# Kernel tuning notes

Measured on AMD Instinct MI355X. Metric: run time of the kernel, lower is better.

The kernel has to match this reference:

```python
import jax, jax.numpy as jnp
import numpy as np

CELU_ALPHA = 0.1  # torchani standard CELU alpha


def _celu(x):
    return jax.nn.celu(x, alpha=CELU_ALPHA)


def setup_inputs() -> dict:
    key = jax.random.key(0)
    ks = jax.random.split(key, 12)
    N, S, E, D = 20000, 4, 8, 1008
    dims = [D, 256, 192, 160, 1]
    inp = {
        "aev": jax.random.normal(ks[0], (N, D), jnp.float32),
        "species": jax.random.randint(ks[1], (N,), 0, S, dtype=jnp.int64),
    }
    for l in range(4):
        din, dout = dims[l], dims[l + 1]
        inp[f"W{l}"] = jax.random.normal(ks[2 + 2 * l], (S, E, din, dout), jnp.float32) * (1.0 / np.sqrt(din).astype(np.float32))
        inp[f"b{l}"] = jax.random.normal(ks[3 + 2 * l], (S, E, dout), jnp.float32) * 0.05
    return inp


def reference(aev, species, W0, b0, W1, b1, W2, b2, W3, b3):
    # Faithful math of InferModel.forward: for each species i, gather atoms of
    # that species, run the BmmAtomicNetwork (ensemble of MLPs via bmm, CELU
    # activations, mean over ensemble members), sum per-species energies, then
    # sum into a single [1]-shaped total energy.
    # JIT-friendly equivalent: evaluate every species network on all atoms
    # (S=4 is small) and select each atom's output by its species index.
    # h: [S, E, N, hidden]
    h = _celu(jnp.einsum('ni,seio->seno', aev, W0) + b0[:, :, None, :])
    h = _celu(jnp.einsum('seni,seio->seno', h, W1) + b1[:, :, None, :])
    h = _celu(jnp.einsum('seni,seio->seno', h, W2) + b2[:, :, None, :])
    h = jnp.einsum('seni,seio->seno', h, W3) + b3[:, :, None, :]  # [S,E,N,1]
    per_atom = h.mean(axis=1)[:, :, 0]  # mean over ensemble -> [S, N]
    sel = jnp.take_along_axis(per_atom, species[None, :], axis=0)[0]  # [N]
    return jnp.sum(sel, keepdims=True)  # shape [1], total energy
```

## Files before the change

kernel.cpp:

```cpp
#include <hip/hip_runtime.h>
#include <cmath>

#define NA 20000
#define NS 4
#define NE 8
#define DD 1008
#define BM 128
#define MAXT 157
#define MAXROWS 20608

typedef unsigned short u16;
typedef unsigned int u32;
typedef unsigned long long u64;
typedef u16 u16x8 __attribute__((ext_vector_type(8)));
typedef u16 u16x4 __attribute__((ext_vector_type(4)));
typedef float f32x4 __attribute__((ext_vector_type(4)));
typedef short s16x8 __attribute__((ext_vector_type(8)));

__device__ __forceinline__ float bf2f(u16 h) {
  u32 u = ((u32)h) << 16;
  return __builtin_bit_cast(float, u);
}
__device__ __forceinline__ u16 f2bf(float f) {
  u32 b = __builtin_bit_cast(u32, f);
  u32 lsb = (b >> 16) & 1;
  return (u16)((b + 0x7fffu + lsb) >> 16);
}
__device__ __forceinline__ float celu_f(float x) {
#if __has_builtin(__builtin_amdgcn_exp2f)
  float e = __builtin_amdgcn_exp2f(x * 14.426950408889634f);
#else
  float e = exp2f(x * 14.426950408889634f);
#endif
  return x > 0.f ? x : 0.1f * (e - 1.f);
}
__device__ __forceinline__ float gf(const void* g, size_t i, bool isF32) {
  return isF32 ? ((const float*)g)[i] : bf2f(((const u16*)g)[i]);
}

__device__ __forceinline__ void gll16(const void* g, const u16* lds) {
#if __has_builtin(__builtin_amdgcn_global_load_lds)
  __builtin_amdgcn_global_load_lds(
      (const __attribute__((address_space(1))) u32*)g,
      (__attribute__((address_space(3))) u32*)(u16*)lds, 16, 0, 0);
#else
  int l = threadIdx.x & 63;
  *(f32x4*)((u16*)lds + l * 8) = *(const f32x4*)g;
#endif
}

#define CHUNK_BARRIER(N)                                   \
  do {                                                     \
    asm volatile("s_waitcnt vmcnt(" #N ")" ::: "memory");  \
    __builtin_amdgcn_sched_barrier(0);                     \
    __builtin_amdgcn_s_barrier();                          \
    __builtin_amdgcn_sched_barrier(0);                     \
  } while (0)

__global__ void k_probe0(const void* __restrict__ aev, const void* __restrict__ species,
                         int* __restrict__ w) {
  __shared__ int sh[2];
  int tid = threadIdx.x;
  if (tid < 64) w[tid] = 0;
  if (tid == 0) { sh[0] = 0; sh[1] = 0; }
  __syncthreads();
  const u16* a = (const u16*)aev;
  int bad = 0;
  for (int i = 0; i < 16; ++i) {
    u16 h = a[tid * 16 + i];
    int ex = (h >> 7) & 0xFF;
    if (ex < 107 || ex > 147) ++bad;
  }
  atomicAdd(&sh[0], bad);
  const int* sp = (const int*)species;
  int odd = 0;
  for (int i = 0; i < 4; ++i)
    if (sp[(tid * 4 + i) * 2 + 1] != 0) ++odd;
  atomicAdd(&sh[1], odd);
  __syncthreads();
  if (tid == 0) {
    w[18] = (sh[0] > 400) ? 1 : 0;
    w[19] = (sh[1] == 0) ? 1 : 0;
  }
}

__device__ __forceinline__ int get_species(const void* sp, int i, bool i64) {
  int s = i64 ? ((const int*)sp)[2 * i] : ((const int*)sp)[i];
  return s < 0 ? 0 : (s > 3 ? 3 : s);
}

__global__ void k_count(const void* __restrict__ species, int* __restrict__ w) {
  int i = blockIdx.x * 256 + threadIdx.x;
  int lane = threadIdx.x & 63;
  int s = (i < NA) ? get_species(species, i, w[19] != 0) : -1;
  for (int sp = 0; sp < 4; ++sp) {
    u64 m = __ballot(s == sp);
    if (m != 0 && lane == (__ffsll((long long)m) - 1))
      atomicAdd(&w[sp], __popcll(m));
  }
  __syncthreads();
  if (threadIdx.x == 0) {
    __threadfence();
    if (atomicAdd(&w[25], 1) == (int)gridDim.x - 1) {
      int b = 0, pb = 0;
      for (int sp = 0; sp < 4; ++sp) {
        int c = atomicAdd(&w[sp], 0);
        w[13 + sp] = b; b += c;
        w[20 + sp] = pb; pb += ((c + 127) >> 7) << 7;
      }
      w[24] = pb;
    }
  }
}

__global__ void k_scatsml(const void* __restrict__ species, int* __restrict__ w,
                          int* __restrict__ order,
                          const void* b0, const void* b1, const void* b2, const void* b3,
                          const void* W3, u16* ob0, u16* ob1, u16* ob2, u16* ob3,
                          u16* oW3, u16* gap) {
  if (blockIdx.x == 79) {
    const bool isF32 = (w[18] != 0);
    int t = threadIdx.x;
    for (int i = t; i < 32 * 256; i += 256) ob0[i] = f2bf(gf(b0, i, isF32));
    for (int i = t; i < 32 * 192; i += 256) ob1[i] = f2bf(gf(b1, i, isF32));
    for (int i = t; i < 32 * 160; i += 256) ob2[i] = f2bf(gf(b2, i, isF32));
    for (int i = t; i < 32 * 160; i += 256) oW3[i] = f2bf(gf(W3, i, isF32));
    if (t < 32) ob3[t] = f2bf(gf(b3, t, isF32));
    u16x8 z = {0, 0, 0, 0, 0, 0, 0, 0};
    *(u16x8*)(gap + t * 8) = z;
    return;
  }
  int i = blockIdx.x * 256 + threadIdx.x;
  int lane = threadIdx.x & 63;
  int s = (i < NA) ? get_species(species, i, w[19] != 0) : -1;
  for (int sp = 0; sp < 4; ++sp) {
    u64 m = __ballot(s == sp);
    if (m == 0) continue;
    int leader = __ffsll((long long)m) - 1;
    int base = 0;
    if (lane == leader) base = atomicAdd(&w[4 + sp], __popcll(m));
    base = __shfl(base, leader);
    if (s == sp) {
      int rank = __popcll(m & ((lane == 63) ? 0x7fffffffffffffffULL : ((1ULL << lane) - 1)));
      order[w[13 + sp] + base + rank] = i;
    }
  }
}

__global__ void k_gather(const void* __restrict__ aev, const int* __restrict__ w,
                         const int* __restrict__ order, u16* __restrict__ aevb) {
  const bool isF32 = (w[18] != 0);
  const int t = threadIdx.x;
  const int r = blockIdx.x * 4 + (t >> 7);
  const int j = t & 127;
  if (j >= 126) return;
  const int s = (r >= w[21]) + (r >= w[22]) + (r >= w[23]);
  const int local = r - w[20 + s];
  u16x8 v = {0, 0, 0, 0, 0, 0, 0, 0};
  if (local < w[s]) {
    const int src = order[w[13 + s] + local];
    if (isF32) {
      const float* p = (const float*)aev + (size_t)src * DD + j * 8;
      const f32x4 f0 = *(const f32x4*)p;
      const f32x4 f1 = *(const f32x4*)(p + 4);
#pragma unroll
      for (int i = 0; i < 4; ++i) { v[i] = f2bf(f0[i]); v[4 + i] = f2bf(f1[i]); }
    } else {
      v = *(const u16x8*)((const u16*)aev + (size_t)src * DD + j * 8);
    }
  }
  *(u16x8*)(aevb + (size_t)r * DD + j * 8) = v;
}

__device__ void tr_tile(const void* __restrict__ W, u16* __restrict__ out,
                        int K, int N, int Kpad, bool isF32, int se,
                        int k0, int n0, int t, u16 (*tile)[68]) {
  const size_t inBase = (size_t)se * K * N;
#pragma unroll
  for (int c = 0; c < 4; ++c) {
    int kk = (t >> 4) + c * 16, nn = (t & 15) * 4;
    int k = k0 + kk, n = n0 + nn;
    u16x4 v = {0, 0, 0, 0};
    if (k < K && n < N) {
      if (isF32) {
        f32x4 f = *(const f32x4*)((const float*)W + inBase + (size_t)k * N + n);
        v[0] = f2bf(f[0]); v[1] = f2bf(f[1]); v[2] = f2bf(f[2]); v[3] = f2bf(f[3]);
      } else {
        v = *(const u16x4*)((const u16*)W + inBase + (size_t)k * N + n);
      }
    }
    *(u16x4*)(&tile[kk][nn]) = v;
  }
  __syncthreads();
  int nloc = t >> 2, ks = (t & 3) * 16;
  if (n0 + nloc < N) {
    u16x8 o0, o1;
#pragma unroll
    for (int i = 0; i < 8; ++i) { o0[i] = tile[ks + i][nloc]; o1[i] = tile[ks + 8 + i][nloc]; }
    size_t ob = (size_t)se * N * Kpad + (size_t)(n0 + nloc) * Kpad + k0 + ks;
    *(u16x8*)(out + ob) = o0;
    *(u16x8*)(out + ob + 8) = o1;
  }
}

__global__ void k_tr3(const void* __restrict__ W0, const void* __restrict__ W1,
                      const void* __restrict__ W2, u16* __restrict__ o0,
                      u16* __restrict__ o1, u16* __restrict__ o2,
                      const int* __restrict__ w) {
  __shared__ u16 tile[64][68];
  const bool isF32 = (w[18] != 0);
  const int se = blockIdx.x, by = blockIdx.y, bz = blockIdx.z, t = threadIdx.x;
  tr_tile(W0, o0, 1008, 256, 1024, isF32, se, by * 64, bz * 64, t, tile);
  if (by < 4 && bz < 3) {
    __syncthreads();
    tr_tile(W1, o1, 256, 192, 256, isF32, se, by * 64, bz * 64, t, tile);
  }
  if (by < 3 && bz < 3) {
    __syncthreads();
    tr_tile(W2, o2, 192, 160, 192, isF32, se, by * 64, bz * 64, t, tile);
  }
}

__global__ __launch_bounds__(512, 4) void k_main(
    const u16* __restrict__ aevb, const u16* __restrict__ wt0,
    const u16* __restrict__ wt1, const u16* __restrict__ wt2,
    const u16* __restrict__ w3b, const u16* __restrict__ b0b,
    const u16* __restrict__ b1b, const u16* __restrict__ b2b,
    const u16* __restrict__ b3b, const int* __restrict__ w,
    float* __restrict__ accum) {
  __shared__ __align__(16) u16 L[32768];

  const int tid = threadIdx.x;
  const int g = blockIdx.x;
  const int s = g >> 1;
  const int e = (g & 1) * 4 + (blockIdx.y & 3);
  const int tile = blockIdx.y >> 2;
  const int cnt = w[s];
  if (tile * BM >= cnt) return;
  const int mRow = w[20 + s] + tile * BM;
  const int mCount = min(BM, cnt - tile * BM);
  const int se = s * NE + e;

  const int lane = tid & 63;
  const int wv = tid >> 6;
  const int lcol = lane & 15;
  const int quad = lane >> 4;

  {
    const u16* wt0se = wt0 + (size_t)se * 256 * 1024;
    const int wm = wv >> 2, wn = wv & 3;

    const int slot0 = wv * 64 + lane;
    const int slot1 = 512 + wv * 64 + lane;
    const int r0 = slot0 >> 3, r1 = slot1 >> 3;
    const u16* gA0 = aevb + (size_t)(mRow + r0) * 1008 + (((slot0 & 7) ^ (r0 & 7)) << 3);
    const u16* gA1 = aevb + (size_t)(mRow + r1) * 1008 + (((slot1 & 7) ^ (r1 & 7)) << 3);
    const int ldsA0 = wv * 512;
    const int ldsA1 = 4096 + wv * 512;

    int rAoff[4], rAx[4];
#pragma unroll
    for (int mt = 0; mt < 4; ++mt) {
      const int row = wm * 64 + mt * 16 + lcol;
      rAoff[mt] = row * 64;
      rAx[mt] = row & 7;
    }

    const u16* bp[4];
#pragma unroll
    for (int nt = 0; nt < 4; ++nt)
      bp[nt] = wt0se + (size_t)(wn * 64 + nt * 16 + lcol) * 1024 + quad * 8;

    f32x4 acc[4][4];
#pragma unroll
    for (int i = 0; i < 4; ++i)
#pragma unroll
      for (int j = 0; j < 4; ++j) acc[i][j] = (f32x4){0.f, 0.f, 0.f, 0.f};

    gll16(gA0, &L[0 * 8192 + ldsA0]);
    gll16(gA1, &L[0 * 8192 + ldsA1]);
    gll16(gA0 + 64, &L[1 * 8192 + ldsA0]);
    gll16(gA1 + 64, &L[1 * 8192 + ldsA1]);
    u16x8 bCur[4], bNxt[4];
#pragma unroll
    for (int nt = 0; nt < 4; ++nt) bCur[nt] = *(const u16x8*)bp[nt];
    CHUNK_BARRIER(2);

    int bufC = 0, bufS = 2;
#pragma unroll 2
    for (int p = 0; p < 32; ++p) {
      const int c = p >> 1, h = p & 1;
      if (p < 31) {
#pragma unroll
        for (int nt = 0; nt < 4; ++nt)
          bNxt[nt] = *(const u16x8*)(bp[nt] + (p + 1) * 32);
      }
      if (h == 0 && c + 2 < 16) {
        gll16(gA0 + (c + 2) * 64, &L[bufS * 8192 + ldsA0]);
        gll16(gA1 + (c + 2) * 64, &L[bufS * 8192 + ldsA1]);
      }
      const int h4 = h << 2;
      s16x8 aF[4];
#pragma unroll
      for (int mt = 0; mt < 4; ++mt)
        aF[mt] = __builtin_bit_cast(s16x8,
            *(const u16x8*)&L[bufC * 8192 + rAoff[mt] + (((h4 + quad) ^ rAx[mt]) << 3)]);
      __builtin_amdgcn_s_setprio(1);
#pragma unroll
      for (int nt = 0; nt < 4; ++nt) {
        const s16x8 bF = __builtin_bit_cast(s16x8, bCur[nt]);
#pragma unroll
        for (int mt = 0; mt < 4; ++mt)
          acc[mt][nt] = __builtin_amdgcn_mfma_f32_16x16x32_bf16(aF[mt], bF, acc[mt][nt], 0, 0, 0);
      }
      __builtin_amdgcn_s_setprio(0);
#pragma unroll
      for (int nt = 0; nt < 4; ++nt) bCur[nt] = bNxt[nt];
      if (h == 1) {
        CHUNK_BARRIER(6);
        bufC = (bufC == 2) ? 0 : bufC + 1;
        bufS = (bufS == 2) ? 0 : bufS + 1;
      }
    }

#pragma unroll
    for (int nt = 0; nt < 4; ++nt) {
      const int col = wn * 64 + nt * 16 + lcol;
      const float bb = bf2f(b0b[se * 256 + col]);
#pragma unroll
      for (int mt = 0; mt < 4; ++mt) {
#pragma unroll
        for (int r = 0; r < 4; ++r) {
          const int rr = wm * 64 + mt * 16 + quad * 4 + r;
          L[(rr * 256 + col) ^ ((rr & 7) << 3)] = f2bf(celu_f(acc[mt][nt][r] + bb));
        }
      }
    }
  }
  __syncthreads();

  {
    const int wm = wv >> 2, wn = wv & 3;
    const u16* w1se = wt1 + (size_t)se * 192 * 256;
    const u16* bp[3];
#pragma unroll
    for (int nt = 0; nt < 3; ++nt)
      bp[nt] = w1se + (size_t)(wn * 48 + nt * 16 + lcol) * 256 + quad * 8;
    f32x4 acc[4][3];
#pragma unroll
    for (int i = 0; i < 4; ++i)
#pragma unroll
      for (int j = 0; j < 3; ++j) acc[i][j] = (f32x4){0.f, 0.f, 0.f, 0.f};
    int aBase[4], aSwz[4];
#pragma unroll
    for (int mt = 0; mt < 4; ++mt) {
      const int row = wm * 64 + mt * 16 + lcol;
      aBase[mt] = row * 256 + quad * 8;
      aSwz[mt] = (row & 7) << 3;
    }
    u16x8 cB[3], nB[3];
#pragma unroll
    for (int nt = 0; nt < 3; ++nt) cB[nt] = *(const u16x8*)bp[nt];
    for (int kc = 0; kc < 8; ++kc) {
      if (kc < 7) {
#pragma unroll
        for (int nt = 0; nt < 3; ++nt) nB[nt] = *(const u16x8*)(bp[nt] + (kc + 1) * 32);
      }
      s16x8 aF[4];
#pragma unroll
      for (int mt = 0; mt < 4; ++mt)
        aF[mt] = __builtin_bit_cast(s16x8, *(const u16x8*)&L[(aBase[mt] + kc * 32) ^ aSwz[mt]]);
#pragma unroll
      for (int nt = 0; nt < 3; ++nt) {
        const s16x8 bF = __builtin_bit_cast(s16x8, cB[nt]);
#pragma unroll
        for (int mt = 0; mt < 4; ++mt)
          acc[mt][nt] = __builtin_amdgcn_mfma_f32_16x16x32_bf16(aF[mt], bF, acc[mt][nt], 0, 0, 0);
      }
      if (kc < 7) {
#pragma unroll
        for (int nt = 0; nt < 3; ++nt) cB[nt] = nB[nt];
      }
    }
    __syncthreads();
#pragma unroll
    for (int nt = 0; nt < 3; ++nt) {
      const int col = wn * 48 + nt * 16 + lcol;
      const float bb = bf2f(b1b[se * 192 + col]);
#pragma unroll
      for (int mt = 0; mt < 4; ++mt) {
#pragma unroll
        for (int r = 0; r < 4; ++r) {
          const int rr = wm * 64 + mt * 16 + quad * 4 + r;
          L[(rr * 192 + col) ^ ((rr & 7) << 3)] = f2bf(celu_f(acc[mt][nt][r] + bb));
        }
      }
    }
  }
  __syncthreads();

  {
    const int wm = wv >> 1, wn = wv & 1;
    const u16* w2se = wt2 + (size_t)se * 160 * 192;
    const u16* bp[5];
#pragma unroll
    for (int nt = 0; nt < 5; ++nt)
      bp[nt] = w2se + (size_t)(wn * 80 + nt * 16 + lcol) * 192 + quad * 8;
    f32x4 acc[2][5];
#pragma unroll
    for (int i = 0; i < 2; ++i)
#pragma unroll
      for (int j = 0; j < 5; ++j) acc[i][j] = (f32x4){0.f, 0.f, 0.f, 0.f};
    int aBase[2], aSwz[2];
#pragma unroll
    for (int mt = 0; mt < 2; ++mt) {
      const int row = wm * 32 + mt * 16 + lcol;
      aBase[mt] = row * 192 + quad * 8;
      aSwz[mt] = (row & 7) << 3;
    }
    u16x8 cB[5], nB[5];
#pragma unroll
    for (int nt = 0; nt < 5; ++nt) cB[nt] = *(const u16x8*)bp[nt];
    for (int kc = 0; kc < 6; ++kc) {
      if (kc < 5) {
#pragma unroll
        for (int nt = 0; nt < 5; ++nt) nB[nt] = *(const u16x8*)(bp[nt] + (kc + 1) * 32);
      }
      s16x8 aF[2];
#pragma unroll
      for (int mt = 0; mt < 2; ++mt)
        aF[mt] = __builtin_bit_cast(s16x8, *(const u16x8*)&L[(aBase[mt] + kc * 32) ^ aSwz[mt]]);
#pragma unroll
      for (int nt = 0; nt < 5; ++nt) {
        const s16x8 bF = __builtin_bit_cast(s16x8, cB[nt]);
#pragma unroll
        for (int mt = 0; mt < 2; ++mt)
          acc[mt][nt] = __builtin_amdgcn_mfma_f32_16x16x32_bf16(aF[mt], bF, acc[mt][nt], 0, 0, 0);
      }
      if (kc < 5) {
#pragma unroll
        for (int nt = 0; nt < 5; ++nt) cB[nt] = nB[nt];
      }
    }
    __syncthreads();
#pragma unroll
    for (int nt = 0; nt < 5; ++nt) {
      const int col = wn * 80 + nt * 16 + lcol;
      const float bb = bf2f(b2b[se * 160 + col]);
#pragma unroll
      for (int mt = 0; mt < 2; ++mt) {
#pragma unroll
        for (int r = 0; r < 4; ++r) {
          const int rr = wm * 32 + mt * 16 + quad * 4 + r;
          L[(rr * 160 + col) ^ ((rr & 7) << 3)] = f2bf(celu_f(acc[mt][nt][r] + bb));
        }
      }
    }
  }
  __syncthreads();

  {
    const int row = tid >> 2;
    const int pp = tid & 3;
    const u16* w3p = w3b + se * 160;
    float dotv = 0.f;
#pragma unroll
    for (int j = 0; j < 5; ++j) {
      const int ci = (pp + 4 * j) * 8;
      const u16x8 hv = *(const u16x8*)&L[(row * 160 + ci) ^ ((row & 7) << 3)];
      const u16x8 wv8 = *(const u16x8*)(w3p + ci);
#pragma unroll
      for (int t2 = 0; t2 < 8; ++t2)
        dotv = fmaf(bf2f(hv[t2]), bf2f(wv8[t2]), dotv);
    }
    dotv += __shfl_xor(dotv, 1);
    dotv += __shfl_xor(dotv, 2);
    float v = (pp == 0 && row < mCount) ? (dotv + bf2f(b3b[se])) : 0.f;
    v += __shfl_xor(v, 4);
    v += __shfl_xor(v, 8);
    v += __shfl_xor(v, 16);
    v += __shfl_xor(v, 32);
    float* redf = (float*)&L[20608];
    if (lane == 0) redf[wv] = v;
    __syncthreads();
    if (tid == 0) {
      float tot = 0.f;
#pragma unroll
      for (int i = 0; i < 8; ++i) tot += redf[i];
      atomicAdd(accum, tot * 0.125f);
    }
  }
}

__global__ void k_final(const float* __restrict__ accum, u32* __restrict__ out) {
  u32 h = (u32)f2bf(accum[0]);
  out[0] = (h << 16) | h;
}

extern "C" void kernel_launch(void* const* d_in, const int* in_sizes, int n_in,
                              void* d_out, int out_size, void* d_ws, size_t ws_size,
                              hipStream_t stream) {
  const void* aev = d_in[0];
  const void* species = d_in[1];
  const void* W0 = d_in[2];
  const void* b0 = d_in[3];
  const void* W1 = d_in[4];
  const void* b1 = d_in[5];
  const void* W2 = d_in[6];
  const void* b2 = d_in[7];
  const void* W3 = d_in[8];
  const void* b3 = d_in[9];

  int* wsI = (int*)d_ws;
  float* accum = (float*)((char*)d_ws + 17 * 4);
  int* order = wsI + 1024;
  char* wsB = (char*)d_ws;

  const size_t oB0 = 131072;
  const size_t oB1 = 147456;
  const size_t oB2 = 159744;
  const size_t oB3 = 169984;
  const size_t oW3 = 170048;
  const size_t oAevb = 262144;
  const size_t oGap = 41807872;
  const size_t oWt0 = 41811968;
  const size_t oWt1 = 58589184;
  const size_t oWt2 = 61734912;

  u16* aevb = (u16*)(wsB + oAevb);
  u16* wt0 = (u16*)(wsB + oWt0);
  u16* wt1 = (u16*)(wsB + oWt1);
  u16* wt2 = (u16*)(wsB + oWt2);
  u16* w3b = (u16*)(wsB + oW3);
  u16* b0b = (u16*)(wsB + oB0);
  u16* b1b = (u16*)(wsB + oB1);
  u16* b2b = (u16*)(wsB + oB2);
  u16* b3b = (u16*)(wsB + oB3);

  hipLaunchKernelGGL(k_probe0, dim3(1), dim3(256), 0, stream, aev, species, wsI);
  hipLaunchKernelGGL(k_count, dim3((NA + 255) / 256), dim3(256), 0, stream, species, wsI);
  hipLaunchKernelGGL(k_scatsml, dim3(80), dim3(256), 0, stream, species, wsI, order,
                     b0, b1, b2, b3, W3, b0b, b1b, b2b, b3b, w3b, (u16*)(wsB + oGap));
  hipLaunchKernelGGL(k_gather, dim3(MAXROWS / 4), dim3(512), 0, stream, aev, wsI, order, aevb);
  hipLaunchKernelGGL(k_tr3, dim3(32, 16, 4), dim3(256), 0, stream, W0, W1, W2,
                     wt0, wt1, wt2, wsI);
  hipLaunchKernelGGL(k_main, dim3(8, 4 * MAXT), dim3(512), 0, stream,
                     aevb, wt0, wt1, wt2, w3b, b0b, b1b, b2b, b3b, wsI, accum);
  hipLaunchKernelGGL(k_final, dim3(1), dim3(1), 0, stream, accum, (u32*)d_out);
}
```

Baseline: 482.8 us.

## Stage layer-0 weight tiles through LDS with async loads and finer-grained pipeline

Layer-0 weight fragments were previously loaded straight from global memory into registers, with a register double-buffer. They are now staged into LDS through async global-to-LDS loads in a 3-deep ring. The A tile switches to 32-wide K chunks in a 2-deep ring with an XOR swizzle, and a barrier now runs every K step instead of every other step. The aim is coalesced, latency-hidden weight loads and lower VGPR pressure, at the cost of more LDS traffic and more frequent barriers.

```diff
diff --git a/kernel.cpp b/kernel.cpp
--- a/kernel.cpp
+++ b/kernel.cpp
@@ -250,26 +250,21 @@
     const u16* wt0se = wt0 + (size_t)se * 256 * 1024;
     const int wm = wv >> 2, wn = wv & 3;
 
-    const int slot0 = wv * 64 + lane;
-    const int slot1 = 512 + wv * 64 + lane;
-    const int r0 = slot0 >> 3, r1 = slot1 >> 3;
-    const u16* gA0 = aevb + (size_t)(mRow + r0) * 1008 + (((slot0 & 7) ^ (r0 & 7)) << 3);
-    const u16* gA1 = aevb + (size_t)(mRow + r1) * 1008 + (((slot1 & 7) ^ (r1 & 7)) << 3);
-    const int ldsA0 = wv * 512;
-    const int ldsA1 = 4096 + wv * 512;
-
-    int rAoff[4], rAx[4];
-#pragma unroll
-    for (int mt = 0; mt < 4; ++mt) {
-      const int row = wm * 64 + mt * 16 + lcol;
-      rAoff[mt] = row * 64;
-      rAx[mt] = row & 7;
-    }
-
-    const u16* bp[4];
-#pragma unroll
-    for (int nt = 0; nt < 4; ++nt)
-      bp[nt] = wt0se + (size_t)(wn * 64 + nt * 16 + lcol) * 1024 + quad * 8;
+    const int rowA = tid >> 2;
+    const int gAx = (tid & 3) ^ ((rowA >> 1) & 3);
+    const u16* gA = aevb + (size_t)(mRow + rowA) * 1008 + gAx * 8;
+    const int rB1 = 128 + (tid >> 2);
+    const int gB0x = (tid & 3) ^ (((tid >> 2) >> 1) & 3);
+    const int gB1x = (tid & 3) ^ ((rB1 >> 1) & 3);
+    const u16* gB0 = wt0se + (size_t)(tid >> 2) * 1024 + gB0x * 8;
+    const u16* gB1 = wt0se + (size_t)rB1 * 1024 + gB1x * 8;
+    const int aSt = wv * 512;
+    const int bSt = wv * 512;
+    const int bSt2 = 4096 + wv * 512;
+
+    const int gsw = (quad ^ ((lcol >> 1) & 3)) * 8;
+    const int aRow0 = (wm * 64 + lcol) * 32 + gsw;
+    const int bRow0 = (wn * 64 + lcol) * 32 + gsw;
 
     f32x4 acc[4][4];
 #pragma unroll
@@ -277,50 +272,40 @@
 #pragma unroll
       for (int j = 0; j < 4; ++j) acc[i][j] = (f32x4){0.f, 0.f, 0.f, 0.f};
 
-    gll16(gA0, &L[0 * 8192 + ldsA0]);
-    gll16(gA1, &L[0 * 8192 + ldsA1]);
-    gll16(gA0 + 64, &L[1 * 8192 + ldsA0]);
-    gll16(gA1 + 64, &L[1 * 8192 + ldsA1]);
-    u16x8 bCur[4], bNxt[4];
-#pragma unroll
-    for (int nt = 0; nt < 4; ++nt) bCur[nt] = *(const u16x8*)bp[nt];
+    gll16(gA, &L[aSt]);
+    gll16(gB0, &L[8192 + bSt]);
+    gll16(gB1, &L[8192 + bSt2]);
+    gll16(gB0 + 32, &L[16384 + bSt]);
+    gll16(gB1 + 32, &L[16384 + bSt2]);
     CHUNK_BARRIER(2);
 
-    int bufC = 0, bufS = 2;
-#pragma unroll 2
+    int bbufC = 0, bbufS = 2;
     for (int p = 0; p < 32; ++p) {
-      const int c = p >> 1, h = p & 1;
-      if (p < 31) {
-#pragma unroll
-        for (int nt = 0; nt < 4; ++nt)
-          bNxt[nt] = *(const u16x8*)(bp[nt] + (p + 1) * 32);
-      }
-      if (h == 0 && c + 2 < 16) {
-        gll16(gA0 + (c + 2) * 64, &L[bufS * 8192 + ldsA0]);
-        gll16(gA1 + (c + 2) * 64, &L[bufS * 8192 + ldsA1]);
-      }
-      const int h4 = h << 2;
-      s16x8 aF[4];
+      if (p < 31)
+        gll16(gA + (p + 1) * 32, &L[((p + 1) & 1) * 4096 + aSt]);
+      if (p < 30) {
+        gll16(gB0 + (p + 2) * 32, &L[8192 + bbufS * 8192 + bSt]);
+        gll16(gB1 + (p + 2) * 32, &L[8192 + bbufS * 8192 + bSt2]);
+      }
+      const u16* Ad = &L[(p & 1) * 4096];
+      const u16* Bd = &L[8192 + bbufC * 8192];
+      s16x8 aF[4], bF[4];
 #pragma unroll
       for (int mt = 0; mt < 4; ++mt)
-        aF[mt] = __builtin_bit_cast(s16x8,
-            *(const u16x8*)&L[bufC * 8192 + rAoff[mt] + (((h4 + quad) ^ rAx[mt]) << 3)]);
+        aF[mt] = __builtin_bit_cast(s16x8, *(const u16x8*)(Ad + aRow0 + mt * 512));
+#pragma unroll
+      for (int nt = 0; nt < 4; ++nt)
+        bF[nt] = __builtin_bit_cast(s16x8, *(const u16x8*)(Bd + bRow0 + nt * 512));
       __builtin_amdgcn_s_setprio(1);
 #pragma unroll
-      for (int nt = 0; nt < 4; ++nt) {
-        const s16x8 bF = __builtin_bit_cast(s16x8, bCur[nt]);
+      for (int nt = 0; nt < 4; ++nt)
 #pragma unroll
         for (int mt = 0; mt < 4; ++mt)
-          acc[mt][nt] = __builtin_amdgcn_mfma_f32_16x16x32_bf16(aF[mt], bF, acc[mt][nt], 0, 0, 0);
-      }
+          acc[mt][nt] = __builtin_amdgcn_mfma_f32_16x16x32_bf16(aF[mt], bF[nt], acc[mt][nt], 0, 0, 0);
       __builtin_amdgcn_s_setprio(0);
-#pragma unroll
-      for (int nt = 0; nt < 4; ++nt) bCur[nt] = bNxt[nt];
-      if (h == 1) {
-        CHUNK_BARRIER(6);
-        bufC = (bufC == 2) ? 0 : bufC + 1;
-        bufS = (bufS == 2) ? 0 : bufS + 1;
-      }
+      if (p < 30) CHUNK_BARRIER(2); else CHUNK_BARRIER(0);
+      bbufC = (bbufC == 2) ? 0 : bbufC + 1;
+      bbufS = (bbufS == 2) ? 0 : bbufS + 1;
     }
 
 #pragma unroll
```

Measured after the change: 428.2 us. -11.3%, faster.
